# Kernel optimization log

Measured on AMD Instinct MI355X. Metric: run time of the kernel, lower is better.

## Reference

```python
import jax, jax.numpy as jnp
from jax import lax
import numpy as np

CH = 16      # channel_n
HID = 128    # update MLP width


def setup_inputs() -> dict:
    key = jax.random.key(0)
    ks = jax.random.split(key, 7)
    B, H, W = 4, 224, 224
    x = jax.random.uniform(ks[0], (B, CH, H, W), dtype=jnp.float32)
    # perception: Conv2d(16 -> 48, 3x3, pad 1, no bias), OIHW
    w_percep = jax.random.normal(ks[1], (CH * 3, CH, 3, 3), jnp.float32) * 0.05
    # update MLP: 1x1 convs == pointwise linears over channels
    w1 = jax.random.normal(ks[2], (HID, CH * 3), jnp.float32) * 0.05
    b1 = jax.random.normal(ks[3], (HID,), jnp.float32) * 0.01
    w2 = jax.random.normal(ks[4], (HID, HID), jnp.float32) * 0.05
    b2 = jax.random.normal(ks[5], (HID,), jnp.float32) * 0.01
    w3 = jax.random.normal(ks[6], (CH, HID), jnp.float32) * 0.05  # no bias
    return {"x": x, "w_percep": w_percep, "w1": w1, "b1": b1,
            "w2": w2, "b2": b2, "w3": w3, "steps": 40}


def reference(x, w_percep, w1, b1, w2, b2, w3, steps):
    dn = ("NCHW", "OIHW", "NCHW")

    def step(x, _):
        # 3x3 perception conv, same padding  -> [B, 48, H, W]
        p = lax.conv_general_dilated(x, w_percep, (1, 1), "SAME",
                                     dimension_numbers=dn)
        # pointwise conv-MLP (1x1 convs as channel einsums)
        h = jax.nn.relu(jnp.einsum("bchw,oc->bohw", p, w1) + b1[None, :, None, None])
        h = jax.nn.relu(jnp.einsum("bchw,oc->bohw", h, w2) + b2[None, :, None, None])
        dx = jnp.einsum("bchw,oc->bohw", h, w3)
        # residual update + clamp to [0, 1] (eval mode: no fire mask)
        return jnp.clip(x + dx, 0.0, 1.0), None

    x, _ = lax.scan(step, x, None, length=steps)
    return x
```

## Files before the change

kernel.cpp:

```cpp
#include <hip/hip_runtime.h>


typedef __attribute__((ext_vector_type(8))) short short8;
typedef __attribute__((ext_vector_type(4))) float float4v;

#define MFMA16(a, b, c) __builtin_amdgcn_mfma_f32_16x16x32_bf16((a), (b), (c), 0, 0, 0)

__device__ __forceinline__ short f2bf(float f) {
  unsigned u = __builtin_bit_cast(unsigned, f);
  return (short)((u + 0x8000u) >> 16);
}

__device__ __forceinline__ void async16(const void* g, void* l) {
  __builtin_amdgcn_global_load_lds((const __attribute__((address_space(1))) void*)g,
                                   (__attribute__((address_space(3))) void*)l,
                                   16, 0, 0);
}

#define WS_WE    0
#define WS_W2    43008
#define WS_W3    77824
#define WS_B1    82944
#define WS_B2    83456
#define WS_X32A  83968
#define WS_X32B  12929024
#define WS_X16A  25774080
#define WS_X16B  32196608

__global__ void prep_x(const float* __restrict__ x, float* __restrict__ x32,
                       short* __restrict__ x16) {
  int i = blockIdx.x * 256 + threadIdx.x;
  int w = i % 224;
  int h = (i / 224) % 224;
  int c = (i / 50176) & 15;
  int bb = i / 802816;
  float v = x[i];
  int o = ((bb * 224 + h) * 224 + w) * 16 + c;
  x32[o] = v;
  x16[o] = f2bf(v);
}

__global__ void prep_w(const float* __restrict__ wp, const float* __restrict__ w1,
                       const float* __restrict__ b1, const float* __restrict__ w2,
                       const float* __restrict__ b2, const float* __restrict__ w3,
                       short* __restrict__ wE, short* __restrict__ w2t,
                       short* __restrict__ w3t, float* __restrict__ b1p,
                       float* __restrict__ b2p) {
  int i = blockIdx.x * 256 + threadIdx.x;
  if (i < 21504) {
    int o = i / 168, k = i % 168;
    float v = 0.f;
    if (k < 144) {
      int off = k >> 4, c = k & 15;
      for (int c3 = 0; c3 < 48; ++c3)
        v += w1[o * 48 + c3] * wp[c3 * 144 + c * 9 + off];
    }
    wE[i] = f2bf(v);
  } else if (i < 38912) {
    int j = i - 21504;
    int n = j / 136, kk = j % 136;
    float v = 0.f;
    if (kk < 128) { int ch = 16 * (kk & 7) + (kk >> 3); v = w2[n * 128 + ch]; }
    w2t[j] = f2bf(v);
  } else if (i < 41472) {
    int j = i - 38912;
    float v = 0.f;
    if (j < 2176) {
      int n = j / 136, kk = j % 136;
      if (kk < 128) { int ch = 16 * (kk & 7) + (kk >> 3); v = w3[n * 128 + ch]; }
    }
    w3t[j] = f2bf(v);
  } else if (i < 41600) {
    int p = i - 41472;
    b1p[p] = b1[16 * (p & 7) + (p >> 3)];
  } else {
    int p = i - 41600;
    b2p[p] = b2[16 * (p & 7) + (p >> 3)];
  }
}

template <bool LAST>
__global__ __launch_bounds__(512, 2) void ca_step(
    const short* __restrict__ wEg, const short* __restrict__ w2g,
    const short* __restrict__ w3g, const float* __restrict__ b1p,
    const float* __restrict__ b2p, const float* __restrict__ xs32,
    const short* __restrict__ xs16, float* __restrict__ xd32,
    short* __restrict__ xd16, float* __restrict__ dout) {
  __shared__ short sXH[6 * 3616];
  __shared__ short sBUF[2 * 4 * 2176];
  __shared__ short sH2[4 * 2176];

  const int tid = threadIdx.x;
  const int lane = tid & 63;
  const int wv = tid >> 6;
  const int c16 = lane & 15;
  const int q = lane >> 4;
  const int q8 = q * 8;
  const int qh = q >> 1;
  const int c0 = (q & 1) * 8;

  const int blk = blockIdx.x;
  const int b = blk / 56;
  const int h0 = (blk % 56) * 4;

  const short8 z8 = {0, 0, 0, 0, 0, 0, 0, 0};
  for (int t = wv; t < 42; t += 8) {
    int hr = t / 7, ck = t % 7;
    int hh = h0 - 1 + hr;
    char* l = (char*)sXH + hr * 7232 + 32 + ck * 1024;
    if (hh >= 0 && hh < 224) {
      const char* g = (const char*)xs16 + ((size_t)(b * 224 + hh) * 224) * 32 + ck * 1024;
      async16(g + lane * 16, l);
    } else {
      *(short8*)(l + lane * 16) = z8;
    }
  }
  if (tid < 24) {
    int hr = tid >> 2, wch = tid & 3;
    int colb = (wch < 2) ? 0 : 225;
    *(short8*)((char*)sXH + hr * 7232 + colb * 32 + (wch & 1) * 16) = z8;
  }

  if (wv < 4) {
    short8 wf[5][8];
#pragma unroll
    for (int kc = 0; kc < 5; ++kc)
#pragma unroll
      for (int nt = 0; nt < 8; ++nt)
        wf[kc][nt] = *(const short8*)(wEg + (nt * 16 + c16) * 168 + kc * 32 + q8);
    const float4v bA = *(const float4v*)(b1p + c16 * 8);
    const float4v bB = *(const float4v*)(b1p + c16 * 8 + 4);

    __syncthreads();

    for (int j = 0; j < 15; ++j) {
      if (j < 14) {
        const int t = 4 * j + wv;
        const int rr = t / 14, cb = (t % 14) * 16;
        const int hbase = (rr * 226 + cb) * 16;
        float4v acc[8];
#pragma unroll
        for (int nt = 0; nt < 8; ++nt) acc[nt] = (float4v){0.f, 0.f, 0.f, 0.f};
#pragma unroll
        for (int kc = 0; kc < 5; ++kc) {
          int off = kc * 2 + qh;
          if (off > 8) off = 8;
          int dy = (off * 11) >> 5;
          int dxx = off - dy * 3;
          short8 a = *(const short8*)(sXH + hbase + (dy * 226 + dxx + c16) * 16 + c0);
#pragma unroll
          for (int nt = 0; nt < 8; ++nt) acc[nt] = MFMA16(a, wf[kc][nt], acc[nt]);
        }
        short* dst = sBUF + (j & 1) * 8704 + wv * 2176;
#pragma unroll
        for (int r = 0; r < 4; ++r) {
          short8 pk;
#pragma unroll
          for (int nt = 0; nt < 8; ++nt) {
            float v = acc[nt][r] + ((nt < 4) ? bA[nt] : bB[nt - 4]);
            pk[nt] = f2bf(fmaxf(v, 0.f));
          }
          *(short8*)(dst + (q * 4 + r) * 136 + c16 * 8) = pk;
        }
      }
      __syncthreads();
    }
  } else {
    short8 w2f[4][8];
    short8 w3f[4];
#pragma unroll
    for (int kc = 0; kc < 4; ++kc)
#pragma unroll
      for (int nt = 0; nt < 8; ++nt)
        w2f[kc][nt] = *(const short8*)(w2g + (nt * 16 + c16) * 136 + kc * 32 + q8);
#pragma unroll
    for (int kc = 0; kc < 4; ++kc)
      w3f[kc] = *(const short8*)(w3g + c16 * 136 + kc * 32 + q8);
    const float4v bA = *(const float4v*)(b2p + c16 * 8);
    const float4v bB = *(const float4v*)(b2p + c16 * 8 + 4);

    const int g = wv - 4;
    short* scr = sH2 + g * 2176;

    __syncthreads();

    for (int j = 0; j < 15; ++j) {
      if (j >= 1) {
        const int t = 4 * (j - 1) + g;
        const short* src = sBUF + ((j - 1) & 1) * 8704 + g * 2176;
        float4v acc2[8];
#pragma unroll
        for (int nt = 0; nt < 8; ++nt) acc2[nt] = (float4v){0.f, 0.f, 0.f, 0.f};
#pragma unroll
        for (int kc = 0; kc < 4; ++kc) {
          short8 a = *(const short8*)(src + c16 * 136 + kc * 32 + q8);
#pragma unroll
          for (int nt = 0; nt < 8; ++nt) acc2[nt] = MFMA16(a, w2f[kc][nt], acc2[nt]);
        }
#pragma unroll
        for (int r = 0; r < 4; ++r) {
          short8 pk;
#pragma unroll
          for (int nt = 0; nt < 8; ++nt) {
            float v = acc2[nt][r] + ((nt < 4) ? bA[nt] : bB[nt - 4]);
            pk[nt] = f2bf(fmaxf(v, 0.f));
          }
          *(short8*)(scr + (q * 4 + r) * 136 + c16 * 8) = pk;
        }
        float4v acc3 = (float4v){0.f, 0.f, 0.f, 0.f};
#pragma unroll
        for (int kc = 0; kc < 4; ++kc) {
          short8 a = *(const short8*)(scr + c16 * 136 + kc * 32 + q8);
          acc3 = MFMA16(a, w3f[kc], acc3);
        }
        const int rr = t / 14, cb = (t % 14) * 16;
        const int hglob = h0 + rr;
#pragma unroll
        for (int r = 0; r < 4; ++r) {
          int col = cb + q * 4 + r;
          size_t pix = (size_t)(b * 224 + hglob) * 224 + col;
          float v = xs32[pix * 16 + c16] + acc3[r];
          v = fminf(fmaxf(v, 0.f), 1.f);
          if (LAST) {
            dout[((size_t)(b * 16 + c16) * 224 + hglob) * 224 + col] = v;
          } else {
            xd32[pix * 16 + c16] = v;
            xd16[pix * 16 + c16] = f2bf(v);
          }
        }
      }
      __syncthreads();
    }
  }
}

extern "C" void kernel_launch(void* const* d_in, const int* in_sizes, int n_in,
                              void* d_out, int out_size, void* d_ws, size_t ws_size,
                              hipStream_t stream) {
  const float* x  = (const float*)d_in[0];
  const float* wp = (const float*)d_in[1];
  const float* w1 = (const float*)d_in[2];
  const float* b1 = (const float*)d_in[3];
  const float* w2 = (const float*)d_in[4];
  const float* b2 = (const float*)d_in[5];
  const float* w3 = (const float*)d_in[6];

  char* ws = (char*)d_ws;
  short* wEg = (short*)(ws + WS_WE);
  short* w2g = (short*)(ws + WS_W2);
  short* w3g = (short*)(ws + WS_W3);
  float* b1p = (float*)(ws + WS_B1);
  float* b2p = (float*)(ws + WS_B2);
  float* X32[2] = {(float*)(ws + WS_X32A), (float*)(ws + WS_X32B)};
  short* X16[2] = {(short*)(ws + WS_X16A), (short*)(ws + WS_X16B)};

  prep_x<<<12544, 256, 0, stream>>>(x, X32[0], X16[0]);
  prep_w<<<163, 256, 0, stream>>>(wp, w1, b1, w2, b2, w3, wEg, w2g, w3g, b1p, b2p);

  for (int s = 0; s < 39; ++s) {
    int sb = s & 1;
    ca_step<false><<<224, 512, 0, stream>>>(wEg, w2g, w3g, b1p, b2p,
                                            X32[sb], X16[sb],
                                            X32[1 - sb], X16[1 - sb], nullptr);
  }
  ca_step<true><<<224, 512, 0, stream>>>(wEg, w2g, w3g, b1p, b2p,
                                         X32[1], X16[1],
                                         X32[0], X16[0], (float*)d_out);
}
```

Baseline: 1.146 ms.

## Split layer-3 into its own pipeline stage, prefetch residual, and use a lighter barrier

Adds a third pipeline stage. The layer-2 waves now write a double-buffered H2 tile and run the layer-3 MFMA and residual store one iteration later, which gives 16 loop iterations instead of 15. The fp32 residual value is loaded from global memory at the start of the iteration, before the layer-2 MFMAs, so its latency overlaps compute. __syncthreads is replaced by an inline lgkmcnt(0)+s_barrier that skips waiting on outstanding vector memory ops. This costs more LDS for the extra H2 buffer, which may affect the 2-blocks-per-CU occupancy, plus one extra pipeline iteration.

Result: faster. 1.118 ms (-2.5%).

```diff
diff --git a/kernel.cpp b/kernel.cpp
--- a/kernel.cpp
+++ b/kernel.cpp
@@ -15,6 +15,10 @@
   __builtin_amdgcn_global_load_lds((const __attribute__((address_space(1))) void*)g,
                                    (__attribute__((address_space(3))) void*)l,
                                    16, 0, 0);
+}
+
+__device__ __forceinline__ void sync_lds() {
+  asm volatile("s_waitcnt lgkmcnt(0)\n\ts_barrier" ::: "memory");
 }
 
 #define WS_WE    0
@@ -88,7 +92,7 @@
     short* __restrict__ xd16, float* __restrict__ dout) {
   __shared__ short sXH[6 * 3616];
   __shared__ short sBUF[2 * 4 * 2176];
-  __shared__ short sH2[4 * 2176];
+  __shared__ short sH2[2 * 4 * 2176];
 
   const int tid = threadIdx.x;
   const int lane = tid & 63;
@@ -133,7 +137,7 @@
 
     __syncthreads();
 
-    for (int j = 0; j < 15; ++j) {
+    for (int j = 0; j < 16; ++j) {
       if (j < 14) {
         const int t = 4 * j + wv;
         const int rr = t / 14, cb = (t % 14) * 16;
@@ -163,7 +167,7 @@
           *(short8*)(dst + (q * 4 + r) * 136 + c16 * 8) = pk;
         }
       }
-      __syncthreads();
+      sync_lds();
     }
   } else {
     short8 w2f[4][8];
@@ -180,13 +184,22 @@
     const float4v bB = *(const float4v*)(b2p + c16 * 8 + 4);
 
     const int g = wv - 4;
-    short* scr = sH2 + g * 2176;
 
     __syncthreads();
 
-    for (int j = 0; j < 15; ++j) {
-      if (j >= 1) {
-        const int t = 4 * (j - 1) + g;
+    for (int j = 0; j < 16; ++j) {
+      float xres[4];
+      int rr3 = 0, cb3 = 0, hglob3 = 0;
+      if (j >= 2) {
+        const int t3 = 4 * (j - 2) + g;
+        rr3 = t3 / 14; cb3 = (t3 % 14) * 16; hglob3 = h0 + rr3;
+#pragma unroll
+        for (int r = 0; r < 4; ++r) {
+          size_t pix = (size_t)(b * 224 + hglob3) * 224 + cb3 + q * 4 + r;
+          xres[r] = xs32[pix * 16 + c16];
+        }
+      }
+      if (j >= 1 && j <= 14) {
         const short* src = sBUF + ((j - 1) & 1) * 8704 + g * 2176;
         float4v acc2[8];
 #pragma unroll
@@ -197,6 +210,7 @@
 #pragma unroll
           for (int nt = 0; nt < 8; ++nt) acc2[nt] = MFMA16(a, w2f[kc][nt], acc2[nt]);
         }
+        short* dsth2 = sH2 + ((j & 1) * 4 + g) * 2176;
 #pragma unroll
         for (int r = 0; r < 4; ++r) {
           short8 pk;
@@ -205,31 +219,32 @@
             float v = acc2[nt][r] + ((nt < 4) ? bA[nt] : bB[nt - 4]);
             pk[nt] = f2bf(fmaxf(v, 0.f));
           }
-          *(short8*)(scr + (q * 4 + r) * 136 + c16 * 8) = pk;
-        }
+          *(short8*)(dsth2 + (q * 4 + r) * 136 + c16 * 8) = pk;
+        }
+      }
+      if (j >= 2) {
+        const short* srch2 = sH2 + (((j - 1) & 1) * 4 + g) * 2176;
         float4v acc3 = (float4v){0.f, 0.f, 0.f, 0.f};
 #pragma unroll
         for (int kc = 0; kc < 4; ++kc) {
-          short8 a = *(const short8*)(scr + c16 * 136 + kc * 32 + q8);
+          short8 a = *(const short8*)(srch2 + c16 * 136 + kc * 32 + q8);
           acc3 = MFMA16(a, w3f[kc], acc3);
         }
-        const int rr = t / 14, cb = (t % 14) * 16;
-        const int hglob = h0 + rr;
-#pragma unroll
-        for (int r = 0; r < 4; ++r) {
-          int col = cb + q * 4 + r;
-          size_t pix = (size_t)(b * 224 + hglob) * 224 + col;
-          float v = xs32[pix * 16 + c16] + acc3[r];
+#pragma unroll
+        for (int r = 0; r < 4; ++r) {
+          int col = cb3 + q * 4 + r;
+          size_t pix = (size_t)(b * 224 + hglob3) * 224 + col;
+          float v = xres[r] + acc3[r];
           v = fminf(fmaxf(v, 0.f), 1.f);
           if (LAST) {
-            dout[((size_t)(b * 16 + c16) * 224 + hglob) * 224 + col] = v;
+            dout[((size_t)(b * 16 + c16) * 224 + hglob3) * 224 + col] = v;
           } else {
             xd32[pix * 16 + c16] = v;
             xd16[pix * 16 + c16] = f2bf(v);
           }
         }
       }
-      __syncthreads();
+      sync_lds();
     }
   }
 }
```
